# Performance work log

Hardware: AMD Instinct MI355X
Metric: run time of the kernel (lower is better)

Reference implementation:

```python
import jax, jax.numpy as jnp
import numpy as np

N_NODES = 10000
N_EDGES = 80000
N_GRAPHS = 64
HEADS = 8
F_IN = 128
D1, D2, D3 = 512, 256, 128  # per-head (and output, concat=False) widths
OUT_DIM = 10


def _lin(key, fin, fout):
    kw, kb = jax.random.split(key)
    w = jax.random.normal(kw, (fin, fout), dtype=jnp.float32) * 0.05
    b = jax.random.normal(kb, (fout,), dtype=jnp.float32) * 0.05
    return w, b


def setup_inputs() -> dict:
    key = jax.random.key(0)
    ks = jax.random.split(key, 24)
    x = jax.random.normal(ks[0], (N_NODES, F_IN), dtype=jnp.float32)
    edge_index = jax.random.randint(ks[1], (2, N_EDGES), 0, N_NODES, dtype=jnp.int64)
    batch = jnp.sort(jax.random.randint(ks[2], (N_NODES,), 0, N_GRAPHS, dtype=jnp.int64))
    d = {"x": x, "edge_index": edge_index, "batch": batch}
    # conv1: 128 -> heads*512 (q,k,v), skip 128 -> 512
    d["w_q1"], d["b_q1"] = _lin(ks[3], F_IN, HEADS * D1)
    d["w_k1"], d["b_k1"] = _lin(ks[4], F_IN, HEADS * D1)
    d["w_v1"], d["b_v1"] = _lin(ks[5], F_IN, HEADS * D1)
    d["w_s1"], d["b_s1"] = _lin(ks[6], F_IN, D1)
    # conv2: 512 -> heads*256, skip 512 -> 256
    d["w_q2"], d["b_q2"] = _lin(ks[7], D1, HEADS * D2)
    d["w_k2"], d["b_k2"] = _lin(ks[8], D1, HEADS * D2)
    d["w_v2"], d["b_v2"] = _lin(ks[9], D1, HEADS * D2)
    d["w_s2"], d["b_s2"] = _lin(ks[10], D1, D2)
    # conv3: 256 -> heads*128, skip 256 -> 128
    d["w_q3"], d["b_q3"] = _lin(ks[11], D2, HEADS * D3)
    d["w_k3"], d["b_k3"] = _lin(ks[12], D2, HEADS * D3)
    d["w_v3"], d["b_v3"] = _lin(ks[13], D2, HEADS * D3)
    d["w_s3"], d["b_s3"] = _lin(ks[14], D2, D3)
    # global attention gate + final fc
    d["w_g"], d["b_g"] = _lin(ks[15], D3, 1)
    d["w_fc"], d["b_fc"] = _lin(ks[16], D3, OUT_DIM)
    return d


def _seg_softmax(a, seg, n):
    m = jax.ops.segment_max(a, seg, num_segments=n)
    e = jnp.exp(a - m[seg])
    s = jax.ops.segment_sum(e, seg, num_segments=n)
    return e / (s[seg] + 1e-16)


def _tconv(x, edge_index, wq, bq, wk, bk, wv, bv, ws, bs):
    # PyG TransformerConv, concat=False, root_weight=True, no edge features
    n = x.shape[0]
    c = wq.shape[1] // HEADS
    q = (x @ wq + bq).reshape(n, HEADS, c)
    k = (x @ wk + bk).reshape(n, HEADS, c)
    v = (x @ wv + bv).reshape(n, HEADS, c)
    src, dst = edge_index[0], edge_index[1]
    a = jnp.einsum('ehc,ehc->eh', q[dst], k[src]) / jnp.sqrt(jnp.float32(c))
    alpha = _seg_softmax(a, dst, n)                                  # [E, H]
    out = jax.ops.segment_sum(v[src] * alpha[..., None], dst, num_segments=n)
    return out.mean(axis=1) + (x @ ws + bs)                          # mean over heads + skip


def reference(x, edge_index, batch,
              w_q1, b_q1, w_k1, b_k1, w_v1, b_v1, w_s1, b_s1,
              w_q2, b_q2, w_k2, b_k2, w_v2, b_v2, w_s2, b_s2,
              w_q3, b_q3, w_k3, b_k3, w_v3, b_v3, w_s3, b_s3,
              w_g, b_g, w_fc, b_fc):
    h = jax.nn.elu(_tconv(x, edge_index, w_q1, b_q1, w_k1, b_k1, w_v1, b_v1, w_s1, b_s1))
    h = jax.nn.elu(_tconv(h, edge_index, w_q2, b_q2, w_k2, b_k2, w_v2, b_v2, w_s2, b_s2))
    h = jax.nn.elu(_tconv(h, edge_index, w_q3, b_q3, w_k3, b_k3, w_v3, b_v3, w_s3, b_s3))
    # GlobalAttention pooling: softmax(gate) over nodes within each graph
    gate = h @ w_g + b_g                                             # [N, 1]
    gate = _seg_softmax(gate, batch, N_GRAPHS)
    g = jax.ops.segment_sum(gate * h, batch, num_segments=N_GRAPHS)  # [G, D3]
    return g @ w_fc + b_fc                                           # [G, OUT_DIM]
```

## Files before the change

kernel.cpp:

```cpp
#include <hip/hip_runtime.h>
#include <math.h>

typedef __bf16 bf16;
typedef __bf16 bf16x8 __attribute__((ext_vector_type(8)));
typedef __bf16 bf16x4 __attribute__((ext_vector_type(4)));
typedef __bf16 bf16x2 __attribute__((ext_vector_type(2)));
typedef float f32x4 __attribute__((ext_vector_type(4)));
typedef float f32x2 __attribute__((ext_vector_type(2)));
typedef unsigned int u32;

#define N_NODES 10000
#define N_EDGES 80000
#define N_GRAPHS 64

template<int EPL> struct VecT;
template<> struct VecT<8>{ typedef bf16x8 type; };
template<> struct VecT<4>{ typedef bf16x4 type; };
template<> struct VecT<2>{ typedef bf16x2 type; };

__device__ inline void gload_lds16(const bf16* g, bf16* l){
  __builtin_amdgcn_global_load_lds(
      (const __attribute__((address_space(1))) unsigned int*)g,
      (__attribute__((address_space(3))) unsigned int*)l, 16, 0, 0);
}

__global__ __launch_bounds__(256) void detect_f32_k(const unsigned short* __restrict__ raw, int n,
                                                    int* __restrict__ flagF){
  int i = blockIdx.x*256 + threadIdx.x;
  if (i < n){
    unsigned e = (raw[i] >> 7) & 0xFFu;
    if (e >= 0xC0u) atomicOr(flagF, 1);
  }
}

struct CvPack {
  const void* src[11];
  bf16* dst[11];
  int pre[12];
  int rl[11];
  int st[11];
};
__global__ __launch_bounds__(256) void convert_all(CvPack p, const int* __restrict__ flagF){
  int gid = blockIdx.x*256 + threadIdx.x;
  if (gid >= p.pre[11]) return;
  int t = 0;
  while (gid >= p.pre[t+1]) ++t;
  int i = gid - p.pre[t];
  bool f = (*flagF != 0);
  float v = f ? ((const float*)p.src[t])[i] : (float)((const bf16*)p.src[t])[i];
  int row = i / p.rl[t], col = i - row*p.rl[t];
  p.dst[t][(size_t)row*p.st[t] + col] = (bf16)v;
}

__global__ __launch_bounds__(256) void detect_i64(const int* __restrict__ raw, int* __restrict__ flag){
  int i = blockIdx.x*256 + threadIdx.x;
  if (i < 4000 && raw[2*i+1] != 0) atomicOr(flag, 1);
}

__global__ __launch_bounds__(256) void conv_idx(const int* __restrict__ ei_raw,
                                                const int* __restrict__ b_raw,
                                                const int* __restrict__ flag,
                                                int* __restrict__ src, int* __restrict__ dst,
                                                int* __restrict__ bat, int* __restrict__ cnt){
  int i = blockIdx.x*256 + threadIdx.x;
  bool i32 = (*flag != 0);
  if (i < N_EDGES){
    int s = i32 ? ei_raw[i]   : ei_raw[2*i];
    int d = i32 ? ei_raw[N_EDGES + i] : ei_raw[2*(N_EDGES + i)];
    s = min(max(s, 0), N_NODES-1);
    d = min(max(d, 0), N_NODES-1);
    src[i] = s; dst[i] = d;
    atomicAdd(&cnt[d], 1);
  }
  if (i < N_NODES){
    int b = i32 ? b_raw[i] : b_raw[2*i];
    bat[i] = min(max(b, 0), N_GRAPHS-1);
  }
}

__global__ __launch_bounds__(256) void scanA(const int* __restrict__ cnt, int* __restrict__ fill,
                                             int* __restrict__ bsum, int N){
  __shared__ int s[256];
  int i = blockIdx.x*256 + threadIdx.x;
  int v = (i < N) ? cnt[i] : 0;
  s[threadIdx.x] = v;
  __syncthreads();
  for (int d = 1; d < 256; d <<= 1){
    int t = (threadIdx.x >= d) ? s[threadIdx.x - d] : 0;
    __syncthreads();
    s[threadIdx.x] += t;
    __syncthreads();
  }
  if (i < N) fill[i] = s[threadIdx.x] - v;
  if (threadIdx.x == 255) bsum[blockIdx.x] = s[255];
}
__global__ __launch_bounds__(64) void scanB(int* __restrict__ bsum, int nb){
  if (threadIdx.x == 0){
    int a = 0;
    for (int b = 0; b < nb; ++b){ int t = bsum[b]; bsum[b] = a; a += t; }
  }
}
__global__ __launch_bounds__(256) void scanC(const int* __restrict__ bsum, int* __restrict__ fill,
                                             int* __restrict__ row_ptr, int N){
  int i = blockIdx.x*256 + threadIdx.x;
  if (i < N){
    int st = fill[i] + bsum[i >> 8];
    fill[i] = st;
    row_ptr[i] = st;
  }
  if (i == 0) row_ptr[N] = N_EDGES;
}

__global__ __launch_bounds__(256) void fill_csr(const int* __restrict__ dst,
                                                int* __restrict__ fill, int* __restrict__ eids){
  int e = blockIdx.x*256 + threadIdx.x;
  if (e < N_EDGES){
    int p = atomicAdd(&fill[dst[e]], 1);
    eids[p] = e;
  }
}

__global__ __launch_bounds__(256)
void gemm_bias(const bf16* __restrict__ A, int lda,
               const bf16* __restrict__ Bt,
               const bf16* __restrict__ bias, bf16* __restrict__ Cout, int ldc,
               int M, int N, int K)
{
  __shared__ bf16 As[128*64];
  __shared__ bf16 Bs[128*64];
  const int tid = threadIdx.x;
  const int lane = tid & 63;
  const int wave = tid >> 6;
  const int m0 = blockIdx.y * 128, n0 = blockIdx.x * 128;
  const int wm = (wave >> 1) * 64, wn = (wave & 1) * 64;
  const int l15 = lane & 15, l4 = lane >> 4;
  const int srow = lane >> 3;
  const int schunk = lane & 7;

  f32x4 acc[4][4] = {};

  for (int k0 = 0; k0 < K; k0 += 64){
    #pragma unroll
    for (int j = 0; j < 4; ++j){
      int r0 = (wave*4 + j)*8;
      int r  = r0 + srow;
      int gc = schunk ^ (r & 7);
      int ga = m0 + r; if (ga >= M) ga = M-1;
      gload_lds16(A  + (size_t)ga*lda      + k0 + gc*8, As + r0*64);
      gload_lds16(Bt + (size_t)(n0 + r)*K  + k0 + gc*8, Bs + r0*64);
    }
    __syncthreads();
    #pragma unroll
    for (int kt = 0; kt < 2; ++kt){
      bf16x8 af[4], bfr[4];
      #pragma unroll
      for (int mt = 0; mt < 4; ++mt){
        int row = wm + mt*16 + l15;
        int p = (kt*4 + l4) ^ (l15 & 7);
        af[mt] = *(const bf16x8*)(As + row*64 + p*8);
      }
      #pragma unroll
      for (int nt = 0; nt < 4; ++nt){
        int row = wn + nt*16 + l15;
        int p = (kt*4 + l4) ^ (l15 & 7);
        bfr[nt] = *(const bf16x8*)(Bs + row*64 + p*8);
      }
      #pragma unroll
      for (int mt = 0; mt < 4; ++mt)
        #pragma unroll
        for (int nt = 0; nt < 4; ++nt)
          acc[mt][nt] = __builtin_amdgcn_mfma_f32_16x16x32_bf16(af[mt], bfr[nt], acc[mt][nt], 0, 0, 0);
    }
    __syncthreads();
  }

  #pragma unroll
  for (int nt = 0; nt < 4; ++nt){
    int col = n0 + wn + nt*16 + l15;
    float bv = (float)bias[col];
    #pragma unroll
    for (int mt = 0; mt < 4; ++mt){
      int rbase = m0 + wm + mt*16 + l4*4;
      #pragma unroll
      for (int r = 0; r < 4; ++r){
        int row = rbase + r;
        if (row < M) Cout[(size_t)row*ldc + col] = (bf16)(acc[mt][nt][r] + bv);
      }
    }
  }
}

__global__ __launch_bounds__(512, 1)
void gemm8p_bias(const bf16* __restrict__ A, int lda,
                 const bf16* __restrict__ Bt,
                 const bf16* __restrict__ bias, bf16* __restrict__ Cout, int ldc,
                 int M, int K)
{
  __shared__ bf16 As[3][256*64];
  __shared__ bf16 Bs[3][128*64];
  const int tid = threadIdx.x;
  const int lane = tid & 63;
  const int wave = tid >> 6;
  const int m0 = blockIdx.y * 256, n0 = blockIdx.x * 128;
  const int wm = (wave >> 1) * 64;
  const int wn = (wave & 1) * 64;
  const int l15 = lane & 15, l4 = lane >> 4;
  const int srow = lane >> 3;
  const int schunk = lane & 7;
  const int NT = K >> 6;

  auto stageA = [&](int t, int j){
    int b = t % 3;
    int r0 = (wave + j*8)*8;
    int r  = r0 + srow;
    int gc = schunk ^ srow;
    int ga = m0 + r; if (ga >= M) ga = M-1;
    gload_lds16(A + (size_t)ga*lda + t*64 + gc*8, &As[b][r0*64]);
  };
  auto stageB = [&](int t, int j){
    int b = t % 3;
    int r0 = (wave + j*8)*8;
    int r  = r0 + srow;
    int gc = schunk ^ srow;
    gload_lds16(Bt + (size_t)(n0 + r)*K + t*64 + gc*8, &Bs[b][r0*64]);
  };

  stageA(0,0); stageA(0,1); stageA(0,2); stageA(0,3); stageB(0,0); stageB(0,1);
  if (NT > 1){ stageA(1,0); stageA(1,1); stageA(1,2); stageA(1,3); stageB(1,0); stageB(1,1); }
  if (NT > 1) asm volatile("s_waitcnt vmcnt(6)" ::: "memory");
  else        asm volatile("s_waitcnt vmcnt(0)" ::: "memory");
  __builtin_amdgcn_s_barrier();

  f32x4 acc[4][4] = {};

  for (int t = 0; t < NT; ++t){
    const bf16* as = &As[t % 3][0];
    const bf16* bs = &Bs[t % 3][0];
    bf16x8 bfr[4][2];
    bf16x8 af[2][2];

    #pragma unroll
    for (int nt2 = 0; nt2 < 4; ++nt2)
      #pragma unroll
      for (int kt = 0; kt < 2; ++kt){
        int row = wn + nt2*16 + l15;
        int p = (kt*4 + l4) ^ (l15 & 7);
        bfr[nt2][kt] = *(const bf16x8*)(bs + row*64 + p*8);
      }
    #pragma unroll
    for (int i = 0; i < 2; ++i)
      #pragma unroll
      for (int kt = 0; kt < 2; ++kt){
        int row = wm + i*16 + l15;
        int p = (kt*4 + l4) ^ (l15 & 7);
        af[i][kt] = *(const bf16x8*)(as + row*64 + p*8);
      }
    if (t + 2 < NT){ stageA(t+2,0); stageA(t+2,1); stageB(t+2,0); }
    __builtin_amdgcn_s_setprio(1);
    #pragma unroll
    for (int i = 0; i < 2; ++i)
      #pragma unroll
      for (int nt2 = 0; nt2 < 4; ++nt2)
        #pragma unroll
        for (int kt = 0; kt < 2; ++kt)
          acc[i][nt2] = __builtin_amdgcn_mfma_f32_16x16x32_bf16(af[i][kt], bfr[nt2][kt], acc[i][nt2], 0, 0, 0);
    __builtin_amdgcn_s_setprio(0);

    #pragma unroll
    for (int i = 0; i < 2; ++i)
      #pragma unroll
      for (int kt = 0; kt < 2; ++kt){
        int row = wm + (2+i)*16 + l15;
        int p = (kt*4 + l4) ^ (l15 & 7);
        af[i][kt] = *(const bf16x8*)(as + row*64 + p*8);
      }
    if (t + 2 < NT){ stageA(t+2,2); stageA(t+2,3); stageB(t+2,1); }
    __builtin_amdgcn_s_setprio(1);
    #pragma unroll
    for (int i = 0; i < 2; ++i)
      #pragma unroll
      for (int nt2 = 0; nt2 < 4; ++nt2)
        #pragma unroll
        for (int kt = 0; kt < 2; ++kt)
          acc[2+i][nt2] = __builtin_amdgcn_mfma_f32_16x16x32_bf16(af[i][kt], bfr[nt2][kt], acc[2+i][nt2], 0, 0, 0);
    __builtin_amdgcn_s_setprio(0);

    if (t < NT - 1){
      if (t + 2 < NT) asm volatile("s_waitcnt vmcnt(6)" ::: "memory");
      else            asm volatile("s_waitcnt vmcnt(0)" ::: "memory");
      __builtin_amdgcn_s_barrier();
    }
  }

  #pragma unroll
  for (int nt2 = 0; nt2 < 4; ++nt2){
    int col = n0 + wn + nt2*16 + l15;
    float bv = (float)bias[col];
    #pragma unroll
    for (int mt = 0; mt < 4; ++mt){
      int rbase = m0 + wm + mt*16 + l4*4;
      #pragma unroll
      for (int r = 0; r < 4; ++r){
        int row = rbase + r;
        if (row < M) Cout[(size_t)row*ldc + col] = (bf16)(acc[mt][nt2][r] + bv);
      }
    }
  }
}

template<int BM, int OUTMODE>
__global__ __launch_bounds__(256)
void gemm_fused(const bf16* __restrict__ A, int lda,
                const bf16* __restrict__ Bt,
                const bf16* __restrict__ bp, const bf16* __restrict__ mb,
                const int* __restrict__ row_ptr,
                bf16* __restrict__ outB, int ldo, float* __restrict__ outF,
                int M, int K)
{
  constexpr int PA    = BM/32;
  constexpr int WCOLS = 128/BM;
  constexpr int WTN   = BM;
  constexpr int NT    = WTN/16;
  __shared__ bf16 As[BM*64];
  __shared__ bf16 Bs[128*64];
  const int tid = threadIdx.x;
  const int lane = tid & 63;
  const int wave = tid >> 6;
  const int m0 = blockIdx.y * BM, n0 = blockIdx.x * 128;
  const int wm = (wave / WCOLS) * 32;
  const int wn = (wave % WCOLS) * WTN;
  const int l15 = lane & 15, l4 = lane >> 4;
  const int srow = lane >> 3;
  const int schunk = lane & 7;

  f32x4 acc[2][NT] = {};

  for (int k0 = 0; k0 < K; k0 += 64){
    #pragma unroll
    for (int j = 0; j < PA; ++j){
      int r0 = (wave*PA + j)*8;
      int r  = r0 + srow;
      int gc = schunk ^ (r & 7);
      int ga = m0 + r; if (ga >= M) ga = M-1;
      gload_lds16(A + (size_t)ga*lda + k0 + gc*8, As + r0*64);
    }
    #pragma unroll
    for (int j = 0; j < 4; ++j){
      int r0 = (wave*4 + j)*8;
      int r  = r0 + srow;
      int gc = schunk ^ (r & 7);
      gload_lds16(Bt + (size_t)(n0 + r)*K + k0 + gc*8, Bs + r0*64);
    }
    __syncthreads();
    #pragma unroll
    for (int kt = 0; kt < 2; ++kt){
      bf16x8 af[2], bfr[NT];
      #pragma unroll
      for (int mt = 0; mt < 2; ++mt){
        int row = wm + mt*16 + l15;
        int p = (kt*4 + l4) ^ (l15 & 7);
        af[mt] = *(const bf16x8*)(As + row*64 + p*8);
      }
      #pragma unroll
      for (int nt = 0; nt < NT; ++nt){
        int row = wn + nt*16 + l15;
        int p = (kt*4 + l4) ^ (l15 & 7);
        bfr[nt] = *(const bf16x8*)(Bs + row*64 + p*8);
      }
      #pragma unroll
      for (int mt = 0; mt < 2; ++mt)
        #pragma unroll
        for (int nt = 0; nt < NT; ++nt)
          acc[mt][nt] = __builtin_amdgcn_mfma_f32_16x16x32_bf16(af[mt], bfr[nt], acc[mt][nt], 0, 0, 0);
    }
    __syncthreads();
  }

  if (OUTMODE == 0){
    float bv[NT], mv[NT];
    #pragma unroll
    for (int nt = 0; nt < NT; ++nt){
      int col = n0 + wn + nt*16 + l15;
      bv[nt] = (float)bp[col];
      mv[nt] = (float)mb[col];
    }
    #pragma unroll
    for (int mt = 0; mt < 2; ++mt){
      int rbase = m0 + wm + mt*16 + l4*4;
      #pragma unroll
      for (int r = 0; r < 4; ++r){
        int row = rbase + r;
        if (row < M){
          bool d0 = (row_ptr[row+1] == row_ptr[row]);
          #pragma unroll
          for (int nt = 0; nt < NT; ++nt){
            int col = n0 + wn + nt*16 + l15;
            float v = acc[mt][nt][r] + bv[nt] - (d0 ? mv[nt] : 0.f);
            v = (v > 0.f) ? v : (__expf(v) - 1.f);
            outB[(size_t)row*ldo + col] = (bf16)v;
          }
        }
      }
    }
  } else {
    #pragma unroll
    for (int mt = 0; mt < 2; ++mt){
      int rbase = m0 + wm + mt*16 + l4*4;
      #pragma unroll
      for (int r = 0; r < 4; ++r){
        int row = rbase + r;
        if (row < M){
          #pragma unroll
          for (int nt = 0; nt < NT; ++nt){
            int col = n0 + wn + nt*16 + l15;
            outF[(size_t)row*128 + col] = acc[mt][nt][r];
          }
        }
      }
    }
  }
}

__global__ __launch_bounds__(256)
void finalize_gate(const float* __restrict__ facc, const bf16* __restrict__ bp,
                   const bf16* __restrict__ mb, const int* __restrict__ row_ptr,
                   bf16* __restrict__ hout, const bf16* __restrict__ wg,
                   const bf16* __restrict__ bg, float* __restrict__ gate)
{
  __shared__ float wred[4];
  int idx = blockIdx.x*256 + threadIdx.x;
  int n = idx >> 7, c = idx & 127;
  bool d0 = (row_ptr[n+1] == row_ptr[n]);
  float v = facc[idx] + (float)bp[c] - (d0 ? (float)mb[c] : 0.f);
  v = (v > 0.f) ? v : (__expf(v) - 1.f);
  hout[idx] = (bf16)v;
  float gc = v * (float)wg[c];
  #pragma unroll
  for (int o = 32; o; o >>= 1) gc += __shfl_xor(gc, o, 64);
  int wave = threadIdx.x >> 6;
  if ((threadIdx.x & 63) == 0) wred[wave] = gc;
  __syncthreads();
  if ((threadIdx.x & 127) == 0){
    float g = wred[wave] + wred[wave + 1] + (float)bg[0];
    gate[n] = g;
  }
}

__global__ __launch_bounds__(256)
void pool_graphs(const float* __restrict__ gate, const int* __restrict__ bat,
                 const bf16* __restrict__ h, float* __restrict__ gacc)
{
  int b = blockIdx.x;
  int lo = 0, hi = N_NODES;
  while (lo < hi){ int mid = (lo + hi) >> 1; if (bat[mid] < b) lo = mid + 1; else hi = mid; }
  int s = lo;
  lo = s; hi = N_NODES;
  while (lo < hi){ int mid = (lo + hi) >> 1; if (bat[mid] < b + 1) lo = mid + 1; else hi = mid; }
  int e = lo;

  int t = threadIdx.x;
  float m = -3.4e38f;
  for (int n = s + t; n < e; n += 256) m = fmaxf(m, gate[n]);
  #pragma unroll
  for (int o = 32; o; o >>= 1) m = fmaxf(m, __shfl_xor(m, o, 64));
  __shared__ float red[4];
  int wv = t >> 6;
  if ((t & 63) == 0) red[wv] = m;
  __syncthreads();
  m = fmaxf(fmaxf(red[0], red[1]), fmaxf(red[2], red[3]));

  int team = t >> 7, c = t & 127;
  float acc = 0.f, se = 0.f;
  for (int n = s + team; n < e; n += 2){
    float en = __expf(gate[n] - m);
    acc += en * (float)h[(size_t)n*128 + c];
    if (c == 0) se += en;
  }
  __shared__ float accs[256];
  __shared__ float ses[2];
  accs[t] = acc;
  if (c == 0) ses[team] = se;
  __syncthreads();
  if (t < 128){
    float tot = accs[t] + accs[128 + t];
    float S = ses[0] + ses[1];
    gacc[b*128 + t] = tot / (S + 1e-16f);
  }
}

struct MhPack { const bf16* wk[3]; const bf16* wq[3]; bf16* wzt[3]; int fin[3]; int c[3]; };
__global__ __launch_bounds__(256)
void gemm_mh_all(MhPack P)
{
  const int L = blockIdx.z >> 3, h = blockIdx.z & 7;
  const int Fin = P.fin[L], C = P.c[L];
  const int nb = Fin >> 7;
  if ((int)blockIdx.x >= nb || (int)blockIdx.y >= nb) return;
  __shared__ bf16 As[128*64];
  __shared__ bf16 Bs[128*64];
  const int ld = 8*C;
  const bf16* Ab = P.wk[L] + h*C;
  const bf16* Bb = P.wq[L] + h*C;
  bf16* Cb = P.wzt[L] + (size_t)h*Fin*Fin;
  const int tid = threadIdx.x;
  const int lane = tid & 63;
  const int wave = tid >> 6;
  const int m0 = blockIdx.y * 128, n0 = blockIdx.x * 128;
  const int wm = (wave >> 1) * 64, wn = (wave & 1) * 64;
  const int l15 = lane & 15, l4 = lane >> 4;
  const int srow = lane >> 3;
  const int schunk = lane & 7;

  f32x4 acc[4][4] = {};

  for (int k0 = 0; k0 < C; k0 += 64){
    #pragma unroll
    for (int j = 0; j < 4; ++j){
      int r0 = (wave*4 + j)*8;
      int r  = r0 + srow;
      int gc = schunk ^ (r & 7);
      gload_lds16(Ab + (size_t)(m0 + r)*ld + k0 + gc*8, As + r0*64);
      gload_lds16(Bb + (size_t)(n0 + r)*ld + k0 + gc*8, Bs + r0*64);
    }
    __syncthreads();
    #pragma unroll
    for (int kt = 0; kt < 2; ++kt){
      bf16x8 af[4], bfr[4];
      #pragma unroll
      for (int mt = 0; mt < 4; ++mt){
        int row = wm + mt*16 + l15;
        int p = (kt*4 + l4) ^ (l15 & 7);
        af[mt] = *(const bf16x8*)(As + row*64 + p*8);
      }
      #pragma unroll
      for (int nt = 0; nt < 4; ++nt){
        int row = wn + nt*16 + l15;
        int p = (kt*4 + l4) ^ (l15 & 7);
        bfr[nt] = *(const bf16x8*)(Bs + row*64 + p*8);
      }
      #pragma unroll
      for (int mt = 0; mt < 4; ++mt)
        #pragma unroll
        for (int nt = 0; nt < 4; ++nt)
          acc[mt][nt] = __builtin_amdgcn_mfma_f32_16x16x32_bf16(af[mt], bfr[nt], acc[mt][nt], 0, 0, 0);
    }
    __syncthreads();
  }

  #pragma unroll
  for (int nt = 0; nt < 4; ++nt){
    int col = n0 + wn + nt*16 + l15;
    #pragma unroll
    for (int mt = 0; mt < 4; ++mt){
      int rbase = m0 + wm + mt*16 + l4*4;
      #pragma unroll
      for (int r = 0; r < 4; ++r)
        Cb[(size_t)(rbase + r)*Fin + col] = (bf16)acc[mt][nt][r];
    }
  }
}

struct WvPack { const void* wv[3]; const void* ws[3]; bf16* bt[3]; int fin[3]; int c[3]; int bx[3]; int by[3]; };
__global__ __launch_bounds__(256)
void prep_wv_all(WvPack P, const int* __restrict__ flagF)
{
  const int L = blockIdx.z;
  if ((int)blockIdx.x >= P.bx[L] || (int)blockIdx.y >= P.by[L]) return;
  __shared__ float t[32][33];
  bool f = (*flagF != 0);
  const int Fin = P.fin[L], C = P.c[L];
  int k0 = blockIdx.x*32, j0 = blockIdx.y*32;
  int x = threadIdx.x & 31, y = threadIdx.x >> 5;
  const void* srcp; int nstride, cb; float sc; int i0;
  if (k0 < 8*Fin){
    int h = k0 / Fin; i0 = k0 - h*Fin;
    srcp = P.wv[L]; nstride = 8*C; cb = h*C + j0; sc = 0.125f;
  } else {
    i0 = k0 - 8*Fin;
    srcp = P.ws[L]; nstride = C; cb = j0; sc = 1.0f;
  }
  #pragma unroll
  for (int ii = 0; ii < 4; ++ii){
    int i = i0 + y + ii*8;
    size_t idx = (size_t)i*nstride + cb + x;
    float v = f ? ((const float*)srcp)[idx] : (float)((const bf16*)srcp)[idx];
    t[y + ii*8][x] = v*sc;
  }
  __syncthreads();
  #pragma unroll
  for (int ii = 0; ii < 4; ++ii){
    int j = j0 + y + ii*8;
    P.bt[L][(size_t)j*(9*Fin) + k0 + x] = (bf16)t[x][y + ii*8];
  }
}

struct SmPack { const bf16* wkc[3]; const void* bq[3]; const void* bv[3]; const void* bs[3];
                int fin[3]; int c[3]; bf16* tz[3]; bf16* bp[3]; bf16* mb[3]; int rb[3]; int bpb[3]; };
__global__ __launch_bounds__(256)
void prep_small_all(SmPack P, const int* __restrict__ flagF)
{
  const int L = blockIdx.z;
  const int Fin = P.fin[L], C = P.c[L];
  const int rb = P.rb[L];
  if ((int)blockIdx.x >= rb + P.bpb[L]) return;
  bool f = (*flagF != 0);
  if ((int)blockIdx.x < rb){
    int wave = threadIdx.x >> 6, lane = threadIdx.x & 63;
    int r = blockIdx.x*4 + wave;
    int h = r / Fin, i = r - h*Fin;
    int epc = C >> 6;
    const bf16* wp = P.wkc[L] + (size_t)i*8*C + h*C;
    const void* bqp = P.bq[L];
    float s = 0.f;
    for (int k = 0; k < epc; ++k){
      int c = k*64 + lane;
      float b = f ? ((const float*)bqp)[h*C + c] : (float)((const bf16*)bqp)[h*C + c];
      s += (float)wp[c] * b;
    }
    #pragma unroll
    for (int o = 32; o; o >>= 1) s += __shfl_xor(s, o, 64);
    if (lane == 0) P.tz[L][r] = (bf16)s;
  } else {
    int idx = ((int)blockIdx.x - rb)*256 + threadIdx.x;
    if (idx < C){
      float s = 0.f;
      for (int h = 0; h < 8; ++h)
        s += f ? ((const float*)P.bv[L])[h*C + idx] : (float)((const bf16*)P.bv[L])[h*C + idx];
      s *= 0.125f;
      float bsv = f ? ((const float*)P.bs[L])[idx] : (float)((const bf16*)P.bs[L])[idx];
      P.mb[L][idx] = (bf16)s;
      P.bp[L][idx] = (bf16)(s + bsv);
    }
  }
}

template<int Fin, int NHT>
__global__ __launch_bounds__(256)
void node_edge(const bf16* __restrict__ z, int zw, int hbase,
               bf16* __restrict__ AP, int ldP,
               const int* __restrict__ row_ptr, const int* __restrict__ eids,
               const int* __restrict__ srcv, float scale)
{
  constexpr int EPL  = Fin/64;
  constexpr int EPL2 = EPL/2;
  constexpr int KC   = Fin/32;
  typedef typename VecT<EPL>::type vecb;
  __shared__ float sw[4][68][12];

  const int wave = threadIdx.x >> 6;
  const int lane = threadIdx.x & 63;
  const int n = blockIdx.x*4 + wave;

  const int beg = row_ptr[n];
  int deg = row_ptr[n+1] - beg;
  if (deg > 64) deg = 64;

  bf16* APn = AP + (size_t)n*ldP;

  if (deg == 0){
    vecb zv;
    #pragma unroll
    for (int k = 0; k < EPL; ++k) zv[k] = (bf16)0.f;
    #pragma unroll
    for (int h = 0; h < NHT; ++h)
      *(vecb*)(APn + (size_t)(hbase + h)*Fin + lane*EPL) = zv;
    return;
  }

  int e_ld = (lane < deg) ? lane : 0;
  int srcReg = srcv[eids[beg + e_ld]];

  const int nc = (deg + 15) >> 4;
  const int l15 = lane & 15, l4 = lane >> 4;
  const int h   = l15 & (NHT-1);
  const bf16* zp = z + (size_t)n*zw + (size_t)h*Fin + l4*8;

  f32x4 sacc[4];
  #pragma unroll
  for (int c = 0; c < 4; ++c) sacc[c] = (f32x4){0.f,0.f,0.f,0.f};

  #pragma unroll
  for (int c = 0; c < 4; ++c){
    if (c < nc){
      int sn = __shfl(srcReg, c*16 + l15, 64);
      const bf16* ap = AP + (size_t)sn*ldP + 8*Fin + l4*8;
      f32x4 s = (f32x4){0.f,0.f,0.f,0.f};
      #pragma unroll
      for (int k = 0; k < KC; ++k){
        bf16x8 af = *(const bf16x8*)(ap + k*32);
        bf16x8 bv = *(const bf16x8*)(zp + k*32);
        s = __builtin_amdgcn_mfma_f32_16x16x32_bf16(af, bv, s, 0, 0, 0);
      }
      sacc[c] = s;
    }
  }

  float m = -3.4e38f;
  #pragma unroll
  for (int c = 0; c < 4; ++c){
    if (c < nc){
      #pragma unroll
      for (int r = 0; r < 4; ++r){
        int row = c*16 + l4*4 + r;
        float v = sacc[c][r]*scale;
        sacc[c][r] = v;
        if (row < deg) m = fmaxf(m, v);
      }
    }
  }
  m = fmaxf(m, __shfl_xor(m, 16, 64));
  m = fmaxf(m, __shfl_xor(m, 32, 64));
  float ssum = 0.f;
  #pragma unroll
  for (int c = 0; c < 4; ++c){
    if (c < nc){
      #pragma unroll
      for (int r = 0; r < 4; ++r){
        int row = c*16 + l4*4 + r;
        float e = (row < deg) ? __expf(sacc[c][r] - m) : 0.f;
        sacc[c][r] = e;
        ssum += e;
      }
    }
  }
  ssum += __shfl_xor(ssum, 16, 64);
  ssum += __shfl_xor(ssum, 32, 64);
  float inv = 1.f/(ssum + 1e-16f);

  if (l15 < NHT){
    #pragma unroll
    for (int c = 0; c < 4; ++c){
      if (c < nc){
        #pragma unroll
        for (int r = 0; r < 4; ++r)
          sw[wave][c*16 + l4*4 + r][l15] = sacc[c][r]*inv;
      }
    }
  }
  if (lane < 4*NHT)
    sw[wave][nc*16 + (lane >> 3)][lane & 7] = 0.f;

  f32x2 acc[NHT][EPL2];
  #pragma unroll
  for (int hh = 0; hh < NHT; ++hh)
    #pragma unroll
    for (int p = 0; p < EPL2; ++p) acc[hh][p] = (f32x2){0.f,0.f};

  for (int i0 = 0; i0 < deg; i0 += 4){
    int sn0 = __shfl(srcReg, i0,   64);
    int sn1 = __shfl(srcReg, i0+1, 64);
    int sn2 = __shfl(srcReg, i0+2, 64);
    int sn3 = __shfl(srcReg, i0+3, 64);
    vecb hv0 = *(const vecb*)(AP + (size_t)sn0*ldP + 8*Fin + lane*EPL);
    vecb hv1 = *(const vecb*)(AP + (size_t)sn1*ldP + 8*Fin + lane*EPL);
    vecb hv2 = *(const vecb*)(AP + (size_t)sn2*ldP + 8*Fin + lane*EPL);
    vecb hv3 = *(const vecb*)(AP + (size_t)sn3*ldP + 8*Fin + lane*EPL);
    #pragma unroll
    for (int j = 0; j < 4; ++j){
      int e = i0 + j;
      vecb hv = (j == 0) ? hv0 : (j == 1) ? hv1 : (j == 2) ? hv2 : hv3;
      f32x4 w0 = *(const f32x4*)&sw[wave][e][0];
      f32x4 w1 = (NHT == 8) ? *(const f32x4*)&sw[wave][e][4] : w0;
      f32x2 xf[EPL2];
      const u32* up = (const u32*)&hv;
      #pragma unroll
      for (int p = 0; p < EPL2; ++p){
        u32 u = up[p];
        xf[p] = (f32x2){ __uint_as_float(u << 16), __uint_as_float(u & 0xffff0000u) };
      }
      #pragma unroll
      for (int hh = 0; hh < NHT; ++hh){
        float w = (hh < 4) ? w0[hh] : w1[hh-4];
        f32x2 wv = (f32x2){w, w};
        #pragma unroll
        for (int p = 0; p < EPL2; ++p)
          acc[hh][p] += wv * xf[p];
      }
    }
  }

  #pragma unroll
  for (int hh = 0; hh < NHT; ++hh){
    vecb o;
    #pragma unroll
    for (int p = 0; p < EPL2; ++p){
      o[2*p]   = (bf16)acc[hh][p][0];
      o[2*p+1] = (bf16)acc[hh][p][1];
    }
    *(vecb*)(APn + (size_t)(hbase + hh)*Fin + lane*EPL) = o;
  }
}

__global__ __launch_bounds__(64) void final_fc(const float* __restrict__ gacc, const bf16* __restrict__ wfc,
                                               const bf16* __restrict__ bfc, void* __restrict__ out,
                                               const int* __restrict__ flagF){
  int g = blockIdx.x;
  int o = threadIdx.x;
  if (o < 10){
    float s = (float)bfc[o];
    for (int c = 0; c < 128; ++c) s += gacc[g*128 + c]*(float)wfc[c*10 + o];
    if (*flagF) ((float*)out)[(size_t)g*10 + o] = s;
    else        ((bf16*)out)[(size_t)g*10 + o]  = (bf16)s;
  }
}

extern "C" void kernel_launch(void* const* d_in, const int* in_sizes, int n_in,
                              void* d_out, int out_size, void* d_ws, size_t ws_size,
                              hipStream_t stream)
{
  const int* ei   = (const int*)d_in[1];
  const int* braw = (const int*)d_in[2];

  bf16 *Wzt1=0,*Wzt2=0,*Wzt3=0,*Wvt1=0,*Wvt2=0,*Wvt3=0;
  float *facc=0,*gate=0;
  bf16 *tz1=0,*tz2=0,*tz3=0,*bp1=0,*mb1=0,*bp2=0,*mb2=0,*bp3=0,*mb3=0,*h3=0;
  bf16 *cwg=0,*cbg=0,*cwfc=0,*cbfc=0;
  int *src=0,*dst=0,*bat=0,*cnt=0,*row_ptr=0,*fillp=0,*eids=0,*flagbuf=0;
  char *A1=0, *A2=0;

  auto plan = [&](bool big)->size_t{
    size_t off = 0;
    auto A = [&](size_t bytes)->char*{
      char* p = (char*)d_ws + off;
      off += (bytes + 255) & ~(size_t)255;
      return p;
    };
    A1 = A(92160000);
    A2 = A(big ? 81920000 : 46080000);
    Wzt1 = (bf16*)A((size_t)8*128*128*2);
    Wzt2 = (bf16*)A((size_t)8*512*512*2);
    Wzt3 = (bf16*)A((size_t)8*256*256*2);
    Wvt1 = (bf16*)A((size_t)512*9*128*2);
    Wvt2 = (bf16*)A((size_t)256*9*512*2);
    Wvt3 = (bf16*)A((size_t)128*9*256*2);
    facc = (float*)A((size_t)N_NODES*512*4);
    tz1  = (bf16*)A(8*128*2);
    tz2  = (bf16*)A(8*512*2);
    tz3  = (bf16*)A(8*256*2);
    bp1  = (bf16*)A(512*2);  mb1 = (bf16*)A(512*2);
    bp2  = (bf16*)A(256*2);  mb2 = (bf16*)A(256*2);
    bp3  = (bf16*)A(128*2);  mb3 = (bf16*)A(128*2);
    h3   = (bf16*)A((size_t)N_NODES*128*2);
    src  = (int*)A((size_t)N_EDGES*4);
    dst  = (int*)A((size_t)N_EDGES*4);
    bat  = (int*)A((size_t)N_NODES*4);
    cnt  = (int*)A((size_t)N_NODES*4);
    row_ptr = (int*)A((size_t)(N_NODES+1)*4);
    fillp= (int*)A((size_t)N_NODES*4);
    eids = (int*)A((size_t)N_EDGES*4);
    flagbuf = (int*)A(16384);
    gate = (float*)A((size_t)N_NODES*4);
    unsigned* poolz = (unsigned*)A((size_t)(64 + 64 + 64*128)*4);
    (void)poolz;
    cwg  = (bf16*)A(128*2);
    cbg  = (bf16*)A(2*2);
    cwfc = (bf16*)A(1280*2);
    cbfc = (bf16*)A(10*2);
    return off;
  };

  bool big = (plan(true) <= ws_size);
  if (!big && plan(false) > ws_size) return;
  plan(big);
  unsigned* poolz = (unsigned*)((char*)gate + (((size_t)N_NODES*4 + 255) & ~(size_t)255));

  int* flagI = flagbuf;
  int* flagF = flagbuf + 1;
  int* bsum  = (int*)((char*)flagbuf + 8192);
  float*    gacc = (float*)(poolz + 128);

  bf16* AP1 = (bf16*)A2;   const int ldP1 = 1152;
  bf16* z1  = (bf16*)A1;
  bf16* AP2 = (bf16*)A1;   const int ldP2 = 4608;
  bf16* z2  = (bf16*)A2;
  bf16* AP3 = (bf16*)A2;   const int ldP3 = 2304;
  bf16* z3  = (bf16*)A1;
  bf16* wq1c = (bf16*)(A1 + 48000000);  bf16* wk1c = wq1c + 128*4096;
  bf16* wq2c = wk1c + 128*4096;         bf16* wk2c = wq2c + 512*2048;
  bf16* wq3c = wk2c + 512*2048;         bf16* wk3c = wq3c + 256*1024;

  hipMemsetAsync(flagbuf, 0, 16384, stream);
  {
    int nprobe = in_sizes[0] < 32768 ? in_sizes[0] : 32768;
    detect_f32_k<<<(nprobe + 255)/256, 256, 0, stream>>>((const unsigned short*)d_in[0], nprobe, flagF);
    detect_i64<<<16, 256, 0, stream>>>(ei, flagI);
  }

  {
    CvPack p;
    const int CIDX[11] = {0, 3, 5, 11, 13, 19, 21, 27, 28, 29, 30};
    bf16* CDST[11] = {AP1 + 1024, wq1c, wk1c, wq2c, wk2c, wq3c, wk3c, cwg, cbg, cwfc, cbfc};
    int tot = 0;
    for (int t = 0; t < 11; ++t){
      p.src[t] = d_in[CIDX[t]];
      p.dst[t] = CDST[t];
      p.pre[t] = tot;
      int n = in_sizes[CIDX[t]];
      tot += n;
      if (t == 0){ p.rl[t] = 128; p.st[t] = 1152; }
      else       { p.rl[t] = n;   p.st[t] = n;    }
    }
    p.pre[11] = tot;
    convert_all<<<(tot + 255)/256, 256, 0, stream>>>(p, flagF);
  }

  hipMemsetAsync(cnt, 0, (size_t)N_NODES*4, stream);
  conv_idx<<<(N_EDGES + 255)/256, 256, 0, stream>>>(ei, braw, flagI, src, dst, bat, cnt);
  scanA<<<40, 256, 0, stream>>>(cnt, fillp, bsum, N_NODES);
  scanB<<<1, 64, 0, stream>>>(bsum, 40);
  scanC<<<40, 256, 0, stream>>>(bsum, fillp, row_ptr, N_NODES);
  fill_csr<<<(N_EDGES + 255)/256, 256, 0, stream>>>(dst, fillp, eids);

  {
    MhPack mp;
    mp.wk[0]=wk1c; mp.wk[1]=wk2c; mp.wk[2]=wk3c;
    mp.wq[0]=wq1c; mp.wq[1]=wq2c; mp.wq[2]=wq3c;
    mp.wzt[0]=Wzt1; mp.wzt[1]=Wzt2; mp.wzt[2]=Wzt3;
    mp.fin[0]=128; mp.fin[1]=512; mp.fin[2]=256;
    mp.c[0]=512; mp.c[1]=256; mp.c[2]=128;
    gemm_mh_all<<<dim3(4,4,24), 256, 0, stream>>>(mp);

    WvPack wp;
    wp.wv[0]=d_in[7];  wp.wv[1]=d_in[15]; wp.wv[2]=d_in[23];
    wp.ws[0]=d_in[9];  wp.ws[1]=d_in[17]; wp.ws[2]=d_in[25];
    wp.bt[0]=Wvt1; wp.bt[1]=Wvt2; wp.bt[2]=Wvt3;
    wp.fin[0]=128; wp.fin[1]=512; wp.fin[2]=256;
    wp.c[0]=512; wp.c[1]=256; wp.c[2]=128;
    wp.bx[0]=36; wp.bx[1]=144; wp.bx[2]=72;
    wp.by[0]=16; wp.by[1]=8;   wp.by[2]=4;
    prep_wv_all<<<dim3(144,16,3), 256, 0, stream>>>(wp, flagF);

    SmPack sp;
    sp.wkc[0]=wk1c; sp.wkc[1]=wk2c; sp.wkc[2]=wk3c;
    sp.bq[0]=d_in[4];  sp.bq[1]=d_in[12]; sp.bq[2]=d_in[20];
    sp.bv[0]=d_in[8];  sp.bv[1]=d_in[16]; sp.bv[2]=d_in[24];
    sp.bs[0]=d_in[10]; sp.bs[1]=d_in[18]; sp.bs[2]=d_in[26];
    sp.fin[0]=128; sp.fin[1]=512; sp.fin[2]=256;
    sp.c[0]=512; sp.c[1]=256; sp.c[2]=128;
    sp.tz[0]=tz1; sp.tz[1]=tz2; sp.tz[2]=tz3;
    sp.bp[0]=bp1; sp.bp[1]=bp2; sp.bp[2]=bp3;
    sp.mb[0]=mb1; sp.mb[1]=mb2; sp.mb[2]=mb3;
    sp.rb[0]=256;  sp.rb[1]=1024; sp.rb[2]=512;
    sp.bpb[0]=2;   sp.bpb[1]=1;   sp.bpb[2]=1;
    prep_small_all<<<dim3(1025,1,3), 256, 0, stream>>>(sp, flagF);
  }

  const int MT = (N_NODES + 127)/128;
  const int NB = N_NODES/4;
  const int MT32 = (N_NODES + 31)/32;
  const int MT64 = (N_NODES + 63)/64;
  const int MT256 = (N_NODES + 255)/256;
  const float sc1 = 1.0f/sqrtf(512.f), sc2 = 1.0f/sqrtf(256.f), sc3 = 1.0f/sqrtf(128.f);

  gemm_bias<<<dim3(8, MT), 256, 0, stream>>>(AP1 + 1024, ldP1, Wzt1, tz1, z1, 1024, N_NODES, 1024, 128);
  node_edge<128,8><<<NB, 256, 0, stream>>>(z1, 1024, 0, AP1, ldP1, row_ptr, eids, src, sc1);
  gemm_fused<64,0><<<dim3(4, MT64), 256, 0, stream>>>(AP1, ldP1, Wvt1, bp1, mb1, row_ptr,
                                                      AP2 + 4096, ldP2, (float*)0, N_NODES, 1152);

  if (big){
    gemm8p_bias<<<dim3(32, MT256), 512, 0, stream>>>(AP2 + 4096, ldP2, Wzt2, tz2, z2, 4096, N_NODES, 512);
    node_edge<512,8><<<NB, 256, 0, stream>>>(z2, 4096, 0, AP2, ldP2, row_ptr, eids, src, sc2);
  } else {
    for (int g = 0; g < 2; ++g){
      gemm_bias<<<dim3(16, MT), 256, 0, stream>>>(AP2 + 4096, ldP2, Wzt2 + (size_t)g*4*512*512, tz2 + g*4*512, z2, 2048, N_NODES, 2048, 512);
      node_edge<512,4><<<NB, 256, 0, stream>>>(z2, 2048, g*4, AP2, ldP2, row_ptr, eids, src, sc2);
    }
  }
  gemm_fused<32,0><<<dim3(2, MT32), 256, 0, stream>>>(AP2, ldP2, Wvt2, bp2, mb2, row_ptr,
                                                      AP3 + 2048, ldP3, (float*)0, N_NODES, 4608);

  gemm8p_bias<<<dim3(16, MT256), 512, 0, stream>>>(AP3 + 2048, ldP3, Wzt3, tz3, z3, 2048, N_NODES, 256);
  node_edge<256,8><<<NB, 256, 0, stream>>>(z3, 2048, 0, AP3, ldP3, row_ptr, eids, src, sc3);
  gemm_fused<32,1><<<dim3(1, MT32), 256, 0, stream>>>(AP3, ldP3, Wvt3, (const bf16*)0, (const bf16*)0, (const int*)0,
                                                      (bf16*)0, 0, facc, N_NODES, 2304);
  finalize_gate<<<(N_NODES*128)/256, 256, 0, stream>>>(facc, bp3, mb3, row_ptr, h3, cwg, cbg, gate);

  pool_graphs<<<N_GRAPHS, 256, 0, stream>>>(gate, bat, h3, gacc);
  final_fc<<<N_GRAPHS, 64, 0, stream>>>(gacc, cwfc, cbfc, d_out, flagF);
}
```

Baseline: 554.7 us.

## Add B-resident GEMM for layer-2 projection with per-wave row strips

Adds a GEMM kernel that loads a whole 128-column slice of the weight matrix (K=512) into LDS once per block. Each wave then loops over 64-row strips of A, reading A directly from global memory into registers and issuing MFMAs against the resident B. It replaces the tiled gemm8p_bias for the layer-2 z projection and launches a fixed 32x8 grid, so weight tiles are no longer reloaded for every M tile. In exchange, A is read from global with no LDS staging or double buffering, each wave holds 128 accumulator registers, and the grid has far fewer blocks.

Result: no change. 552.7 us (-0.4%).

```diff
diff --git a/kernel.cpp b/kernel.cpp
--- a/kernel.cpp
+++ b/kernel.cpp
@@ -185,6 +185,84 @@
       for (int r = 0; r < 4; ++r){
         int row = rbase + r;
         if (row < M) Cout[(size_t)row*ldc + col] = (bf16)(acc[mt][nt][r] + bv);
+      }
+    }
+  }
+}
+
+template<int NKB>
+__global__ __launch_bounds__(512, 1)
+void gemm_bres_bias(const bf16* __restrict__ A, int lda,
+                    const bf16* __restrict__ Bt,
+                    const bf16* __restrict__ bias, bf16* __restrict__ Cout, int ldc,
+                    int M, int YB)
+{
+  constexpr int K = NKB*64;
+  __shared__ bf16 Bs[NKB][128*64];
+  const int tid = threadIdx.x;
+  const int lane = tid & 63;
+  const int wave = tid >> 6;
+  const int n0 = blockIdx.x * 128;
+  const int l15 = lane & 15, l4 = lane >> 4;
+  const int srow = lane >> 3;
+  const int schunk = lane & 7;
+
+  #pragma unroll
+  for (int kb = 0; kb < NKB; ++kb){
+    #pragma unroll
+    for (int j = 0; j < 2; ++j){
+      int r0 = (wave*2 + j)*8;
+      int r  = r0 + srow;
+      int gc = schunk ^ srow;
+      gload_lds16(Bt + (size_t)(n0 + r)*K + kb*64 + gc*8, &Bs[kb][r0*64]);
+    }
+  }
+  asm volatile("s_waitcnt vmcnt(0)" ::: "memory");
+  __builtin_amdgcn_s_barrier();
+
+  float bv[8];
+  #pragma unroll
+  for (int nt = 0; nt < 8; ++nt) bv[nt] = (float)bias[n0 + nt*16 + l15];
+
+  const int nstrips = (M + 63) >> 6;
+  const int ws0 = blockIdx.y*8 + wave;
+  const int wstep = YB*8;
+
+  for (int strip = ws0; strip < nstrips; strip += wstep){
+    const int m0 = strip*64;
+    f32x4 acc[4][8] = {};
+    #pragma unroll 2
+    for (int kk = 0; kk < K/32; ++kk){
+      const int kb = kk >> 1, kt = kk & 1;
+      bf16x8 af[4];
+      #pragma unroll
+      for (int mt = 0; mt < 4; ++mt){
+        int row = m0 + mt*16 + l15; if (row >= M) row = M-1;
+        af[mt] = *(const bf16x8*)(A + (size_t)row*lda + kk*32 + l4*8);
+      }
+      bf16x8 bfr[8];
+      #pragma unroll
+      for (int nt = 0; nt < 8; ++nt){
+        int p = (kt*4 + l4) ^ (l15 & 7);
+        bfr[nt] = *(const bf16x8*)(&Bs[kb][(nt*16 + l15)*64 + p*8]);
+      }
+      #pragma unroll
+      for (int mt = 0; mt < 4; ++mt)
+        #pragma unroll
+        for (int nt = 0; nt < 8; ++nt)
+          acc[mt][nt] = __builtin_amdgcn_mfma_f32_16x16x32_bf16(af[mt], bfr[nt], acc[mt][nt], 0, 0, 0);
+    }
+    #pragma unroll
+    for (int mt = 0; mt < 4; ++mt){
+      int rbase = m0 + mt*16 + l4*4;
+      #pragma unroll
+      for (int r = 0; r < 4; ++r){
+        int row = rbase + r;
+        if (row < M){
+          #pragma unroll
+          for (int nt = 0; nt < 8; ++nt)
+            Cout[(size_t)row*ldc + n0 + nt*16 + l15] = (bf16)(acc[mt][nt][r] + bv[nt]);
+        }
       }
     }
   }
@@ -958,7 +1036,7 @@
                                                       AP2 + 4096, ldP2, (float*)0, N_NODES, 1152);
 
   if (big){
-    gemm8p_bias<<<dim3(32, MT256), 512, 0, stream>>>(AP2 + 4096, ldP2, Wzt2, tz2, z2, 4096, N_NODES, 512);
+    gemm_bres_bias<8><<<dim3(32, 8), 512, 0, stream>>>(AP2 + 4096, ldP2, Wzt2, tz2, z2, 4096, N_NODES, 8);
     node_edge<512,8><<<NB, 256, 0, stream>>>(z2, 4096, 0, AP2, ldP2, row_ptr, eids, src, sc2);
   } else {
     for (int g = 0; g < 2; ++g){
```
